# Kernel optimization log

Hardware: AMD Instinct MI355X
Metric: run time of the kernel (lower is better)

The kernel has to match this reference:

```python
import jax, jax.numpy as jnp
import numpy as np

H = 512   # hidden_size
B = 32    # batch
S = 2048  # src_len
NEG = -1e10


def setup_inputs() -> dict:
    key = jax.random.key(0)
    k1, k2, k3, k4, k5, k6 = jax.random.split(key, 6)
    hidden = jax.random.normal(k1, (B, 2 * H), dtype=jnp.float32)
    encoder_outputs = jax.random.normal(k2, (S, B, 2 * H), dtype=jnp.float32)
    mask = jax.random.randint(k3, (B, S), 0, 2, dtype=jnp.int32)
    # params: nn.Linear(4H, H) -> weight [H, 4H], bias [H]; v ~ U[0,1) [H]
    bound = 1.0 / np.sqrt(4 * H)
    attn_w = jax.random.uniform(k4, (H, 4 * H), minval=-bound, maxval=bound, dtype=jnp.float32)
    attn_b = jax.random.uniform(k5, (H,), minval=-bound, maxval=bound, dtype=jnp.float32)
    v = jax.random.uniform(k6, (H,), dtype=jnp.float32)
    return {"hidden": hidden, "encoder_outputs": encoder_outputs, "mask": mask,
            "attn_w": attn_w, "attn_b": attn_b, "v": v}


def reference(hidden, encoder_outputs, mask, attn_w, attn_b, v):
    # hidden: [B, 2H] -> [B, S, 2H]; encoder_outputs: [S, B, 2H] -> [B, S, 2H]
    src_len = encoder_outputs.shape[0]
    h = jnp.broadcast_to(hidden[:, None, :], (hidden.shape[0], src_len, hidden.shape[1]))
    eo = jnp.transpose(encoder_outputs, (1, 0, 2))
    cat = jnp.concatenate((h, eo), axis=2)                      # [B, S, 4H]
    energy = jnp.tanh(jnp.einsum('bsf,hf->bsh', cat, attn_w) + attn_b)  # [B, S, H]
    attention = jnp.einsum('bsh,h->bs', energy, v)              # [B, S]
    attention = jnp.where(mask == 0, NEG, attention)
    return jax.nn.softmax(attention, axis=1)
```

## Files before the change

### kernel.cpp

```cpp
#include <hip/hip_runtime.h>

#define SLEN 2048
#define BATCH 32
#define HDIM 512
#define KDIM 1024

typedef _Float16 f16x8 __attribute__((ext_vector_type(8)));
typedef _Float16 f16x4 __attribute__((ext_vector_type(4)));
typedef float f32x4 __attribute__((ext_vector_type(4)));

__device__ __forceinline__ float fast_tanh(float x) {
  float e = __expf(2.0f * x);
  return 1.0f - 2.0f * __builtin_amdgcn_rcpf(e + 1.0f);
}

__global__ __launch_bounds__(256) void prep_k(const float* __restrict__ attn_w,
                                              const float* __restrict__ attn_b,
                                              const float* __restrict__ hidden,
                                              _Float16* __restrict__ Bt,
                                              float* __restrict__ s1,
                                              float* __restrict__ score) {
  if (blockIdx.x < 512) {
    int t = blockIdx.x * 256 + threadIdx.x;
    int h = t >> 8;
    int c = t & 255;
    float4 x = *(const float4*)(attn_w + (size_t)h * 2048 + 1024 + c * 4);
    f16x4 y = {(_Float16)x.x, (_Float16)x.y, (_Float16)x.z, (_Float16)x.w};
    *(f16x4*)(Bt + (size_t)h * 1024 + c * 4) = y;
  } else if (blockIdx.x < 4608) {
    int o = (blockIdx.x - 512) * 4 + (threadIdx.x >> 6);
    int b = o >> 9, h = o & 511;
    int lane = threadIdx.x & 63;
    const float4* hp = (const float4*)(hidden + (size_t)b * 1024);
    const float4* wp = (const float4*)(attn_w + (size_t)h * 2048);
    float acc = 0.f;
#pragma unroll
    for (int c = 0; c < 4; ++c) {
      float4 a = hp[c * 64 + lane];
      float4 wv = wp[c * 64 + lane];
      acc += a.x * wv.x + a.y * wv.y + a.z * wv.z + a.w * wv.w;
    }
#pragma unroll
    for (int off = 1; off < 64; off <<= 1) acc += __shfl_xor(acc, off);
    if (lane == 0) s1[o] = acc + attn_b[h];
  } else {
    int idx = (blockIdx.x - 4608) * 256 + threadIdx.x;
    float4 z = {0.f, 0.f, 0.f, 0.f};
    ((float4*)score)[idx] = z;
    ((float4*)score)[idx + 8192] = z;
  }
}

__global__ __launch_bounds__(512, 2) void gemm_k(const float* __restrict__ eo,
                                                 const _Float16* __restrict__ Bt,
                                                 const float* __restrict__ s1,
                                                 const float* __restrict__ v,
                                                 float* __restrict__ score) {
  __shared__ __align__(16) char smem[131072];

  int bid = blockIdx.x;
  int x = bid & 7;
  int nt = (bid >> 3) & 3;
  int mt = (bid >> 5) * 8 + x;

  int tid = threadIdx.x;
  int lane = tid & 63;
  int w = tid >> 6;
  int wm = w * 64;
  int mrow = lane & 15;
  int quad = lane >> 4;
  int rk = mrow & 7;

  f32x4 acc[4][8];
#pragma unroll
  for (int i = 0; i < 4; ++i)
#pragma unroll
    for (int j = 0; j < 8; ++j) acc[i][j] = (f32x4){0.f, 0.f, 0.f, 0.f};

#pragma unroll 1
  for (int half = 0; half < 2; ++half) {
    int h0 = half * 512;

    __syncthreads();
    {
      int r = tid >> 2;
      int cg = (tid & 3) * 16;
      const _Float16* src = Bt + (size_t)(nt * 128 + r) * 1024 + h0 + cg * 8;
      char* dst = smem + r * 1024;
#pragma unroll
      for (int c = 0; c < 16; ++c) {
        f16x8 vd = *(const f16x8*)(src + c * 8);
        int pc = (cg + c) ^ (r & 7);
        *(f16x8*)(dst + pc * 16) = vd;
      }
    }
    __syncthreads();

    const float* aB0 = eo + (size_t)(mt * 512 + wm + 0  + mrow) * 1024 + h0 + quad * 8;
    const float* aB1 = eo + (size_t)(mt * 512 + wm + 16 + mrow) * 1024 + h0 + quad * 8;
    const float* aB2 = eo + (size_t)(mt * 512 + wm + 32 + mrow) * 1024 + h0 + quad * 8;
    const float* aB3 = eo + (size_t)(mt * 512 + wm + 48 + mrow) * 1024 + h0 + quad * 8;

#pragma unroll 2
    for (int ks = 0; ks < 16; ++ks) {
      float4 ar0 = *(const float4*)(aB0 + ks * 32);
      float4 ar1 = *(const float4*)(aB0 + ks * 32 + 4);
      float4 ar2 = *(const float4*)(aB1 + ks * 32);
      float4 ar3 = *(const float4*)(aB1 + ks * 32 + 4);
      float4 ar4 = *(const float4*)(aB2 + ks * 32);
      float4 ar5 = *(const float4*)(aB2 + ks * 32 + 4);
      float4 ar6 = *(const float4*)(aB3 + ks * 32);
      float4 ar7 = *(const float4*)(aB3 + ks * 32 + 4);

      int cx = ((ks * 4 + quad) ^ rk) << 4;
      f16x8 bf[8];
#pragma unroll
      for (int j = 0; j < 8; ++j)
        bf[j] = *(const f16x8*)(smem + ((16 * j + mrow) << 10) + cx);

      f16x8 af[4];
      af[0] = (f16x8){(_Float16)ar0.x, (_Float16)ar0.y, (_Float16)ar0.z, (_Float16)ar0.w,
                      (_Float16)ar1.x, (_Float16)ar1.y, (_Float16)ar1.z, (_Float16)ar1.w};
      af[1] = (f16x8){(_Float16)ar2.x, (_Float16)ar2.y, (_Float16)ar2.z, (_Float16)ar2.w,
                      (_Float16)ar3.x, (_Float16)ar3.y, (_Float16)ar3.z, (_Float16)ar3.w};
      af[2] = (f16x8){(_Float16)ar4.x, (_Float16)ar4.y, (_Float16)ar4.z, (_Float16)ar4.w,
                      (_Float16)ar5.x, (_Float16)ar5.y, (_Float16)ar5.z, (_Float16)ar5.w};
      af[3] = (f16x8){(_Float16)ar6.x, (_Float16)ar6.y, (_Float16)ar6.z, (_Float16)ar6.w,
                      (_Float16)ar7.x, (_Float16)ar7.y, (_Float16)ar7.z, (_Float16)ar7.w};

#pragma unroll
      for (int i = 0; i < 4; ++i)
#pragma unroll
        for (int j = 0; j < 8; ++j)
          acc[i][j] = __builtin_amdgcn_mfma_f32_16x16x32_f16(af[i], bf[j], acc[i][j], 0, 0, 0);
    }
  }

  __syncthreads();
  float* s1s = (float*)smem;
  float* vsm = (float*)(smem + 16896);
  for (int t = tid; t < 1024; t += 512) {
    int bb = t >> 5, cc = t & 31;
    ((float4*)s1s)[bb * 33 + cc] = *(const float4*)(s1 + (size_t)bb * 512 + nt * 128 + cc * 4);
  }
  if (tid < 32) ((float4*)vsm)[tid] = *(const float4*)(v + nt * 128 + tid * 4);
  __syncthreads();

  int lcol = mrow;
  float vv[8];
#pragma unroll
  for (int j = 0; j < 8; ++j) vv[j] = vsm[16 * j + lcol];

#pragma unroll
  for (int i = 0; i < 4; ++i) {
#pragma unroll
    for (int r = 0; r < 4; ++r) {
      int mloc = wm + 16 * i + 4 * quad + r;
      int bb = mloc & 31;
      float sum = 0.f;
#pragma unroll
      for (int j = 0; j < 8; ++j) {
        float e = acc[i][j][r] + s1s[bb * 132 + 16 * j + lcol];
        sum += fast_tanh(e) * vv[j];
      }
      sum += __shfl_xor(sum, 1);
      sum += __shfl_xor(sum, 2);
      sum += __shfl_xor(sum, 4);
      sum += __shfl_xor(sum, 8);
      if (lcol == 0) {
        int mg = mt * 512 + mloc;
        atomicAdd(&score[(mg & 31) * SLEN + (mg >> 5)], sum);
      }
    }
  }
}

__global__ __launch_bounds__(256) void softmax_k(const float* __restrict__ score,
                                                 const int* __restrict__ mask,
                                                 float* __restrict__ out) {
  int b = blockIdx.x;
  int tid = threadIdx.x;
  int lane = tid & 63, w = tid >> 6;
  __shared__ float red[8];
  float vals[8];
  float mx = -3.4e38f;
#pragma unroll
  for (int i = 0; i < 8; ++i) {
    int s = i * 256 + tid;
    float xv = score[b * SLEN + s];
    if (mask[b * SLEN + s] == 0) xv = -1e10f;
    vals[i] = xv;
    mx = fmaxf(mx, xv);
  }
#pragma unroll
  for (int off = 1; off < 64; off <<= 1) mx = fmaxf(mx, __shfl_xor(mx, off));
  if (lane == 0) red[w] = mx;
  __syncthreads();
  mx = fmaxf(fmaxf(red[0], red[1]), fmaxf(red[2], red[3]));
  float sum = 0.f;
#pragma unroll
  for (int i = 0; i < 8; ++i) {
    vals[i] = __expf(vals[i] - mx);
    sum += vals[i];
  }
#pragma unroll
  for (int off = 1; off < 64; off <<= 1) sum += __shfl_xor(sum, off);
  if (lane == 0) red[4 + w] = sum;
  __syncthreads();
  sum = red[4] + red[5] + red[6] + red[7];
  float inv = 1.0f / sum;
#pragma unroll
  for (int i = 0; i < 8; ++i) out[b * SLEN + i * 256 + tid] = vals[i] * inv;
}

extern "C" void kernel_launch(void* const* d_in, const int* in_sizes, int n_in,
                              void* d_out, int out_size, void* d_ws, size_t ws_size,
                              hipStream_t stream) {
  const float* hidden = (const float*)d_in[0];
  const float* eo     = (const float*)d_in[1];
  const int*   mask   = (const int*)d_in[2];
  const float* attn_w = (const float*)d_in[3];
  const float* attn_b = (const float*)d_in[4];
  const float* v      = (const float*)d_in[5];
  float* out = (float*)d_out;

  char* wsb = (char*)d_ws;
  _Float16* Bt = (_Float16*)wsb;
  float* s1    = (float*)(wsb + (1 << 20));
  float* score = (float*)(wsb + (1 << 20) + (1 << 16));

  prep_k<<<4640, 256, 0, stream>>>(attn_w, attn_b, hidden, Bt, s1, score);
  gemm_k<<<512, 512, 0, stream>>>(eo, Bt, s1, v, score);
  softmax_k<<<BATCH, 256, 0, stream>>>(score, mask, out);
}
```

Measured before the change: 527.5 us.

## Retile GEMM to full-N per block with async LDS double-buffered A loads

Each block now owns 64 rows of the encoder outputs across all 512 hidden columns, so it writes finished scores directly instead of atomically accumulating partial sums. This also removes the score-zeroing pass from the prep kernel. The A operand (fp32 encoder outputs) is streamed into a small swizzled, double-buffered LDS tile with global_load_lds, while B fragments are read straight from global memory and L2. The block's LDS footprint shrinks so more blocks can be resident, but every block re-reads the whole 1 MB fp16 weight matrix and synchronizes once per 32-wide k step.

Result: faster. 496.7 us (-5.8%).

```diff
diff --git a/kernel.cpp b/kernel.cpp
--- a/kernel.cpp
+++ b/kernel.cpp
@@ -9,6 +9,12 @@
 typedef _Float16 f16x4 __attribute__((ext_vector_type(4)));
 typedef float f32x4 __attribute__((ext_vector_type(4)));
 
+__device__ __forceinline__ void gload16(const void* g, void* l) {
+  __builtin_amdgcn_global_load_lds(
+      (const __attribute__((address_space(1))) unsigned int*)g,
+      (__attribute__((address_space(3))) unsigned int*)l, 16, 0, 0);
+}
+
 __device__ __forceinline__ float fast_tanh(float x) {
   float e = __expf(2.0f * x);
   return 1.0f - 2.0f * __builtin_amdgcn_rcpf(e + 1.0f);
@@ -18,8 +24,7 @@
                                               const float* __restrict__ attn_b,
                                               const float* __restrict__ hidden,
                                               _Float16* __restrict__ Bt,
-                                              float* __restrict__ s1,
-                                              float* __restrict__ score) {
+                                              float* __restrict__ s1) {
   if (blockIdx.x < 512) {
     int t = blockIdx.x * 256 + threadIdx.x;
     int h = t >> 8;
@@ -27,7 +32,7 @@
     float4 x = *(const float4*)(attn_w + (size_t)h * 2048 + 1024 + c * 4);
     f16x4 y = {(_Float16)x.x, (_Float16)x.y, (_Float16)x.z, (_Float16)x.w};
     *(f16x4*)(Bt + (size_t)h * 1024 + c * 4) = y;
-  } else if (blockIdx.x < 4608) {
+  } else {
     int o = (blockIdx.x - 512) * 4 + (threadIdx.x >> 6);
     int b = o >> 9, h = o & 511;
     int lane = threadIdx.x & 63;
@@ -43,135 +48,111 @@
 #pragma unroll
     for (int off = 1; off < 64; off <<= 1) acc += __shfl_xor(acc, off);
     if (lane == 0) s1[o] = acc + attn_b[h];
-  } else {
-    int idx = (blockIdx.x - 4608) * 256 + threadIdx.x;
-    float4 z = {0.f, 0.f, 0.f, 0.f};
-    ((float4*)score)[idx] = z;
-    ((float4*)score)[idx + 8192] = z;
-  }
-}
-
-__global__ __launch_bounds__(512, 2) void gemm_k(const float* __restrict__ eo,
+  }
+}
+
+__global__ __launch_bounds__(512, 4) void gemm_k(const float* __restrict__ eo,
                                                  const _Float16* __restrict__ Bt,
                                                  const float* __restrict__ s1,
                                                  const float* __restrict__ v,
                                                  float* __restrict__ score) {
-  __shared__ __align__(16) char smem[131072];
-
-  int bid = blockIdx.x;
-  int x = bid & 7;
-  int nt = (bid >> 3) & 3;
-  int mt = (bid >> 5) * 8 + x;
-
+  constexpr int NKT = KDIM / 32;
+  __shared__ __align__(16) char smem[16384];
+
+  int mt = blockIdx.x;
   int tid = threadIdx.x;
   int lane = tid & 63;
   int w = tid >> 6;
-  int wm = w * 64;
+  int wn = w * 64;
   int mrow = lane & 15;
   int quad = lane >> 4;
   int rk = mrow & 7;
 
-  f32x4 acc[4][8];
+  const float* ga = eo + (size_t)(mt * 64 + 8 * w + (lane >> 3)) * KDIM
+                       + ((lane & 7) ^ (lane >> 3)) * 4;
+
+  const _Float16* bp0 = Bt + (size_t)(wn + 0  + mrow) * KDIM + quad * 8;
+  const _Float16* bp1 = Bt + (size_t)(wn + 16 + mrow) * KDIM + quad * 8;
+  const _Float16* bp2 = Bt + (size_t)(wn + 32 + mrow) * KDIM + quad * 8;
+  const _Float16* bp3 = Bt + (size_t)(wn + 48 + mrow) * KDIM + quad * 8;
+
+  f32x4 acc[4][4];
 #pragma unroll
   for (int i = 0; i < 4; ++i)
 #pragma unroll
-    for (int j = 0; j < 8; ++j) acc[i][j] = (f32x4){0.f, 0.f, 0.f, 0.f};
+    for (int j = 0; j < 4; ++j) acc[i][j] = (f32x4){0.f, 0.f, 0.f, 0.f};
+
+  gload16(ga, smem + w * 1024);
+  ga += 32;
+  __syncthreads();
 
 #pragma unroll 1
-  for (int half = 0; half < 2; ++half) {
-    int h0 = half * 512;
+  for (int kt = 0; kt < NKT; ++kt) {
+    int cur = kt & 1;
+
+    f16x8 bf0 = *(const f16x8*)(bp0 + kt * 32);
+    f16x8 bf1 = *(const f16x8*)(bp1 + kt * 32);
+    f16x8 bf2 = *(const f16x8*)(bp2 + kt * 32);
+    f16x8 bf3 = *(const f16x8*)(bp3 + kt * 32);
+
+    if (kt + 1 < NKT) {
+      gload16(ga, smem + (cur ^ 1) * 8192 + w * 1024);
+      ga += 32;
+    }
+
+    const float* Ab = (const float*)(smem + cur * 8192);
+    f16x8 af[4];
+#pragma unroll
+    for (int i = 0; i < 4; ++i) {
+      const float* pa = Ab + (16 * i + mrow) * 32;
+      float4 a0 = *(const float4*)(pa + (((2 * quad) ^ rk) << 2));
+      float4 a1 = *(const float4*)(pa + (((2 * quad + 1) ^ rk) << 2));
+      af[i] = (f16x8){(_Float16)a0.x, (_Float16)a0.y, (_Float16)a0.z, (_Float16)a0.w,
+                      (_Float16)a1.x, (_Float16)a1.y, (_Float16)a1.z, (_Float16)a1.w};
+    }
+
+#pragma unroll
+    for (int i = 0; i < 4; ++i) {
+      acc[i][0] = __builtin_amdgcn_mfma_f32_16x16x32_f16(af[i], bf0, acc[i][0], 0, 0, 0);
+      acc[i][1] = __builtin_amdgcn_mfma_f32_16x16x32_f16(af[i], bf1, acc[i][1], 0, 0, 0);
+      acc[i][2] = __builtin_amdgcn_mfma_f32_16x16x32_f16(af[i], bf2, acc[i][2], 0, 0, 0);
+      acc[i][3] = __builtin_amdgcn_mfma_f32_16x16x32_f16(af[i], bf3, acc[i][3], 0, 0, 0);
+    }
 
     __syncthreads();
-    {
-      int r = tid >> 2;
-      int cg = (tid & 3) * 16;
-      const _Float16* src = Bt + (size_t)(nt * 128 + r) * 1024 + h0 + cg * 8;
-      char* dst = smem + r * 1024;
-#pragma unroll
-      for (int c = 0; c < 16; ++c) {
-        f16x8 vd = *(const f16x8*)(src + c * 8);
-        int pc = (cg + c) ^ (r & 7);
-        *(f16x8*)(dst + pc * 16) = vd;
-      }
-    }
-    __syncthreads();
-
-    const float* aB0 = eo + (size_t)(mt * 512 + wm + 0  + mrow) * 1024 + h0 + quad * 8;
-    const float* aB1 = eo + (size_t)(mt * 512 + wm + 16 + mrow) * 1024 + h0 + quad * 8;
-    const float* aB2 = eo + (size_t)(mt * 512 + wm + 32 + mrow) * 1024 + h0 + quad * 8;
-    const float* aB3 = eo + (size_t)(mt * 512 + wm + 48 + mrow) * 1024 + h0 + quad * 8;
-
-#pragma unroll 2
-    for (int ks = 0; ks < 16; ++ks) {
-      float4 ar0 = *(const float4*)(aB0 + ks * 32);
-      float4 ar1 = *(const float4*)(aB0 + ks * 32 + 4);
-      float4 ar2 = *(const float4*)(aB1 + ks * 32);
-      float4 ar3 = *(const float4*)(aB1 + ks * 32 + 4);
-      float4 ar4 = *(const float4*)(aB2 + ks * 32);
-      float4 ar5 = *(const float4*)(aB2 + ks * 32 + 4);
-      float4 ar6 = *(const float4*)(aB3 + ks * 32);
-      float4 ar7 = *(const float4*)(aB3 + ks * 32 + 4);
-
-      int cx = ((ks * 4 + quad) ^ rk) << 4;
-      f16x8 bf[8];
-#pragma unroll
-      for (int j = 0; j < 8; ++j)
-        bf[j] = *(const f16x8*)(smem + ((16 * j + mrow) << 10) + cx);
-
-      f16x8 af[4];
-      af[0] = (f16x8){(_Float16)ar0.x, (_Float16)ar0.y, (_Float16)ar0.z, (_Float16)ar0.w,
-                      (_Float16)ar1.x, (_Float16)ar1.y, (_Float16)ar1.z, (_Float16)ar1.w};
-      af[1] = (f16x8){(_Float16)ar2.x, (_Float16)ar2.y, (_Float16)ar2.z, (_Float16)ar2.w,
-                      (_Float16)ar3.x, (_Float16)ar3.y, (_Float16)ar3.z, (_Float16)ar3.w};
-      af[2] = (f16x8){(_Float16)ar4.x, (_Float16)ar4.y, (_Float16)ar4.z, (_Float16)ar4.w,
-                      (_Float16)ar5.x, (_Float16)ar5.y, (_Float16)ar5.z, (_Float16)ar5.w};
-      af[3] = (f16x8){(_Float16)ar6.x, (_Float16)ar6.y, (_Float16)ar6.z, (_Float16)ar6.w,
-                      (_Float16)ar7.x, (_Float16)ar7.y, (_Float16)ar7.z, (_Float16)ar7.w};
-
-#pragma unroll
-      for (int i = 0; i < 4; ++i)
-#pragma unroll
-        for (int j = 0; j < 8; ++j)
-          acc[i][j] = __builtin_amdgcn_mfma_f32_16x16x32_f16(af[i], bf[j], acc[i][j], 0, 0, 0);
-    }
-  }
-
-  __syncthreads();
-  float* s1s = (float*)smem;
-  float* vsm = (float*)(smem + 16896);
-  for (int t = tid; t < 1024; t += 512) {
-    int bb = t >> 5, cc = t & 31;
-    ((float4*)s1s)[bb * 33 + cc] = *(const float4*)(s1 + (size_t)bb * 512 + nt * 128 + cc * 4);
-  }
-  if (tid < 32) ((float4*)vsm)[tid] = *(const float4*)(v + nt * 128 + tid * 4);
-  __syncthreads();
-
-  int lcol = mrow;
-  float vv[8];
-#pragma unroll
-  for (int j = 0; j < 8; ++j) vv[j] = vsm[16 * j + lcol];
-
+  }
+
+  float vv[4];
+#pragma unroll
+  for (int j = 0; j < 4; ++j) vv[j] = v[wn + 16 * j + mrow];
+
+  float* part = (float*)smem;
 #pragma unroll
   for (int i = 0; i < 4; ++i) {
 #pragma unroll
     for (int r = 0; r < 4; ++r) {
-      int mloc = wm + 16 * i + 4 * quad + r;
-      int bb = mloc & 31;
+      int mloc = 16 * i + 4 * quad + r;
+      int b = mloc & 31;
       float sum = 0.f;
 #pragma unroll
-      for (int j = 0; j < 8; ++j) {
-        float e = acc[i][j][r] + s1s[bb * 132 + 16 * j + lcol];
+      for (int j = 0; j < 4; ++j) {
+        float e = acc[i][j][r] + s1[(size_t)b * 512 + wn + 16 * j + mrow];
         sum += fast_tanh(e) * vv[j];
       }
       sum += __shfl_xor(sum, 1);
       sum += __shfl_xor(sum, 2);
       sum += __shfl_xor(sum, 4);
       sum += __shfl_xor(sum, 8);
-      if (lcol == 0) {
-        int mg = mt * 512 + mloc;
-        atomicAdd(&score[(mg & 31) * SLEN + (mg >> 5)], sum);
-      }
-    }
+      if (mrow == 0) part[w * 64 + mloc] = sum;
+    }
+  }
+  __syncthreads();
+  if (tid < 64) {
+    float s = 0.f;
+#pragma unroll
+    for (int ww = 0; ww < 8; ++ww) s += part[ww * 64 + tid];
+    int mg = mt * 64 + tid;
+    score[(mg & 31) * SLEN + (mg >> 5)] = s;
   }
 }
 
@@ -229,7 +210,7 @@
   float* s1    = (float*)(wsb + (1 << 20));
   float* score = (float*)(wsb + (1 << 20) + (1 << 16));
 
-  prep_k<<<4640, 256, 0, stream>>>(attn_w, attn_b, hidden, Bt, s1, score);
-  gemm_k<<<512, 512, 0, stream>>>(eo, Bt, s1, v, score);
+  prep_k<<<4608, 256, 0, stream>>>(attn_w, attn_b, hidden, Bt, s1);
+  gemm_k<<<1024, 512, 0, stream>>>(eo, Bt, s1, v, score);
   softmax_k<<<BATCH, 256, 0, stream>>>(score, mask, out);
 }
```
